# Optimization experiments

Hardware: AMD Instinct MI355X
Metric: run time of the kernel (lower is better)

## Reference

```python
import jax, jax.numpy as jnp
import numpy as np

VOCAB_SIZE = 8192
EMBED_DIM = 256


def setup_inputs() -> dict:
    key = jax.random.key(0)
    k1, k2 = jax.random.split(key)
    N = 16384  # batch(512) * num_slots(8) * tokens_per_slot(4)
    z = jax.random.normal(k1, (N, EMBED_DIM), dtype=jnp.float32)
    codebook = jax.random.normal(k2, (VOCAB_SIZE, EMBED_DIM), dtype=jnp.float32)
    return {"z": z, "codebook": codebook}


def reference(z, codebook):
    # Squared-distance cdist via the expansion ||z||^2 + ||e||^2 - 2 z.e^T
    z_sq = jnp.sum(z * z, axis=1, keepdims=True)            # [N, 1]
    e_sq = jnp.sum(codebook * codebook, axis=1)              # [V]
    dist = z_sq + e_sq - 2.0 * jnp.matmul(z, codebook.T)     # [N, V]
    tokens = jnp.argmin(dist, axis=-1)                       # [N] int
    z_q = codebook[tokens]                                   # [N, E] gather
    # one-hot reference count (side statistic in the original forward)
    ref_count = jnp.zeros((VOCAB_SIZE,), dtype=jnp.float32).at[tokens].add(1.0)
    return tokens, z_q, ref_count
```

## Files before the change

### kernel.cpp

```cpp
#include <hip/hip_runtime.h>
#include <math.h>

#define N_ROWS 16384
#define VOCAB  8192
#define EMB    256

#define BM 128
#define BV 128
#define BK 64
#define VSPLIT 8
#define VRANGE (VOCAB / VSPLIT)
#define NVT    (VRANGE / BV)
#define TAU 0.15f

typedef _Float16 half8 __attribute__((ext_vector_type(8)));
typedef _Float16 half4 __attribute__((ext_vector_type(4)));
typedef float floatx4 __attribute__((ext_vector_type(4)));

__device__ __forceinline__ void load_lds16(const _Float16* g, _Float16* l) {
    __builtin_amdgcn_global_load_lds(
        (const __attribute__((address_space(1))) void*)g,
        (__attribute__((address_space(3))) void*)l, 16, 0, 0);
}

__global__ void prep_kernel(const float* __restrict__ z, const float* __restrict__ cb,
                            _Float16* __restrict__ zh, _Float16* __restrict__ ch,
                            float* __restrict__ esq, float* __restrict__ cnt,
                            unsigned long long* __restrict__ rkey,
                            int* __restrict__ flagcnt) {
    const int b = blockIdx.x, t = threadIdx.x;
    if (b < VOCAB / 4) {
        const int row  = b * 4 + (t >> 6);
        const int lane = t & 63;
        const float4 f = *(const float4*)(cb + (size_t)row * EMB + lane * 4);
        half4 h;
        h.x = (_Float16)f.x; h.y = (_Float16)f.y; h.z = (_Float16)f.z; h.w = (_Float16)f.w;
        *(half4*)(ch + (size_t)row * EMB + lane * 4) = h;
        float s = f.x * f.x + f.y * f.y + f.z * f.z + f.w * f.w;
        #pragma unroll
        for (int off = 32; off > 0; off >>= 1) s += __shfl_down(s, off, 64);
        if (lane == 0) esq[row] = s;
        if (t < 4) cnt[b * 4 + t] = 0.0f;
        if (t >= 8 && t < 16) rkey[b * 8 + (t - 8)] = ~0ull;
        if (b == 0 && t == 4) flagcnt[0] = 0;
        if (b == 0 && t == 5) flagcnt[1] = 0;
    } else {
        const size_t idx4 = (size_t)(b - VOCAB / 4) * 256 + t;
        const float4 f = *(const float4*)(z + idx4 * 4);
        half4 h;
        h.x = (_Float16)f.x; h.y = (_Float16)f.y; h.z = (_Float16)f.z; h.w = (_Float16)f.w;
        *(half4*)(zh + idx4 * 4) = h;
    }
}

#define KSTEP(KT, RD, WR, LASTSTEP)                                            \
    {                                                                          \
        if (!(LASTSTEP)) {                                                     \
            const _Float16* csn_ = ((KT) < 3) ? csrc : (csrc + (size_t)BV * EMB); \
            const int kon_ = (((KT) + 1) & 3) * BK;                            \
            _Pragma("unroll")                                                  \
            for (int q = 0; q < 4; ++q) {                                      \
                load_lds16(zsrc + (size_t)q * 8 * EMB + kon_,                  \
                           &zs[WR][w * 2048 + q * 512]);                       \
                load_lds16(csn_ + (size_t)q * 8 * EMB + kon_,                  \
                           &cs[WR][w * 2048 + q * 512]);                       \
            }                                                                  \
            asm volatile("s_waitcnt vmcnt(8)" ::: "memory");                   \
        } else {                                                               \
            asm volatile("s_waitcnt vmcnt(0)" ::: "memory");                   \
        }                                                                      \
        __builtin_amdgcn_s_barrier();                                          \
        _Pragma("unroll")                                                      \
        for (int s_ = 0; s_ < 2; ++s_) {                                       \
            const int off_ = s_ ? offA1 : offA0;                               \
            half8 a_[4];                                                       \
            _Pragma("unroll")                                                  \
            for (int i_ = 0; i_ < 4; ++i_)                                     \
                a_[i_] = *(const half8*)&zs[RD][rA[i_] + off_];                \
            _Pragma("unroll")                                                  \
            for (int j_ = 0; j_ < 4; ++j_) {                                   \
                const half8 b_ = *(const half8*)&cs[RD][rB[j_] + off_];        \
                _Pragma("unroll")                                              \
                for (int i_ = 0; i_ < 4; ++i_)                                 \
                    acc[i_][j_] = __builtin_amdgcn_mfma_f32_16x16x32_f16(      \
                        a_[i_], b_, acc[i_][j_], 0, 0, 0);                     \
            }                                                                  \
        }                                                                      \
        __builtin_amdgcn_s_barrier();                                          \
    }

__global__ __launch_bounds__(256, 2)
void mfma_dist_kernel(const _Float16* __restrict__ zh, const _Float16* __restrict__ ch,
                      const float* __restrict__ esq,
                      float* __restrict__ pd1, float* __restrict__ pd2,
                      float* __restrict__ pd3,
                      int* __restrict__ pi1, int* __restrict__ pi2) {
    __shared__ _Float16 zs[2][BM * BK];
    __shared__ _Float16 cs[2][BV * BK];
    float* sc_d1 = (float*)zs;
    float* sc_d2 = sc_d1 + BM * 2;
    float* sc_d3 = sc_d2 + BM * 2;
    int*   sc_i1 = (int*)(sc_d3 + BM * 2);
    int*   sc_i2 = sc_i1 + BM * 2;

    const int row0  = blockIdx.x * BM;
    const int vbase = blockIdx.y * VRANGE;

    const int tid  = threadIdx.x;
    const int w    = tid >> 6;
    const int lane = tid & 63;
    const int lr   = lane & 15;
    const int quad = lane >> 4;
    const int mh   = (w >> 1) * 64;
    const int vh   = (w & 1) * 64;

    const int q7   = quad ^ (lr & 7);
    const int offA0 = q7 * 8;
    const int offA1 = (4 ^ q7) * 8;
    int rA[4], rB[4];
    #pragma unroll
    for (int i = 0; i < 4; ++i) { rA[i] = (mh + i * 16 + lr) * BK; rB[i] = (vh + i * 16 + lr) * BK; }

    const int schunk = (lane & 7) ^ (lane >> 3);
    const _Float16* zsrc = zh + (size_t)(row0 + w * 32 + (lane >> 3)) * EMB + schunk * 8;

    float m1[16], m2[16], m3[16]; int i1[16], i2[16];
    #pragma unroll
    for (int t = 0; t < 16; ++t) {
        m1[t] = -INFINITY; m2[t] = -INFINITY; m3[t] = -INFINITY; i1[t] = 0; i2[t] = 0;
    }

    float ev[4];
    #pragma unroll
    for (int j = 0; j < 4; ++j) ev[j] = esq[vbase + vh + j * 16 + lr];

    {
        const _Float16* csrc0 = ch + (size_t)(vbase + w * 32 + (lane >> 3)) * EMB + schunk * 8;
        #pragma unroll
        for (int q = 0; q < 4; ++q) {
            load_lds16(zsrc  + (size_t)q * 8 * EMB, &zs[0][w * 2048 + q * 512]);
            load_lds16(csrc0 + (size_t)q * 8 * EMB, &cs[0][w * 2048 + q * 512]);
        }
    }

    for (int vt = 0; vt < NVT; ++vt) {
        const int v0 = vbase + vt * BV;
        const _Float16* csrc = ch + (size_t)(v0 + w * 32 + (lane >> 3)) * EMB + schunk * 8;

        floatx4 acc[4][4];
        #pragma unroll
        for (int j = 0; j < 4; ++j) {
            const float e2 = -0.5f * ev[j];
            #pragma unroll
            for (int i = 0; i < 4; ++i) acc[i][j] = (floatx4)e2;
        }
        float evn[4];
        {
            const int vtn = (vt + 1 < NVT) ? vt + 1 : vt;
            #pragma unroll
            for (int j = 0; j < 4; ++j) evn[j] = esq[vbase + vtn * BV + vh + j * 16 + lr];
        }

        KSTEP(0, 0, 1, false)
        KSTEP(1, 1, 0, false)
        KSTEP(2, 0, 1, false)
        KSTEP(3, 1, 0, (vt == NVT - 1))

        int vj[4];
        #pragma unroll
        for (int j = 0; j < 4; ++j) vj[j] = v0 + vh + j * 16 + lr;
        #pragma unroll
        for (int i = 0; i < 4; ++i) {
            #pragma unroll
            for (int reg = 0; reg < 4; ++reg) {
                const int t = i * 4 + reg;
                #pragma unroll
                for (int j = 0; j < 4; ++j) {
                    const float a = acc[i][j][reg];
                    const bool gt1 = a > m1[t];
                    const bool gt2 = a > m2[t];
                    const bool gt3 = a > m3[t];
                    m3[t] = gt2 ? m2[t] : (gt3 ? a : m3[t]);
                    m2[t] = gt1 ? m1[t] : (gt2 ? a : m2[t]);
                    i2[t] = gt1 ? i1[t] : (gt2 ? vj[j] : i2[t]);
                    m1[t] = gt1 ? a : m1[t];
                    i1[t] = gt1 ? vj[j] : i1[t];
                }
            }
        }
        #pragma unroll
        for (int j = 0; j < 4; ++j) ev[j] = evn[j];
    }

    #pragma unroll
    for (int t = 0; t < 16; ++t) {
        float a1 = m1[t], a2 = m2[t], a3 = m3[t]; int ii1 = i1[t], ii2 = i2[t];
        #pragma unroll
        for (int off = 1; off < 16; off <<= 1) {
            const float o1 = __shfl_xor(a1, off, 64);
            const float o2 = __shfl_xor(a2, off, 64);
            const float o3 = __shfl_xor(a3, off, 64);
            const int  oi1 = __shfl_xor(ii1, off, 64);
            const int  oi2 = __shfl_xor(ii2, off, 64);
            const bool g1 = o1 > a1, g2 = o1 > a2, g3 = o1 > a3;
            a3  = g2 ? a2  : (g3 ? o1  : a3);
            a2  = g1 ? a1  : (g2 ? o1  : a2);
            ii2 = g1 ? ii1 : (g2 ? oi1 : ii2);
            a1  = g1 ? o1  : a1;
            ii1 = g1 ? oi1 : ii1;
            const bool h2 = o2 > a2, h3 = o2 > a3;
            a3  = h2 ? a2  : (h3 ? o2 : a3);
            a2  = h2 ? o2  : a2;
            ii2 = h2 ? oi2 : ii2;
            a3 = fmaxf(a3, o3);
        }
        m1[t] = a1; m2[t] = a2; m3[t] = a3; i1[t] = ii1; i2[t] = ii2;
    }
    if (lr == 0) {
        #pragma unroll
        for (int t = 0; t < 16; ++t) {
            const int r = mh + (t >> 2) * 16 + quad * 4 + (t & 3);
            sc_d1[r * 2 + (w & 1)] = m1[t];
            sc_d2[r * 2 + (w & 1)] = m2[t];
            sc_d3[r * 2 + (w & 1)] = m3[t];
            sc_i1[r * 2 + (w & 1)] = i1[t];
            sc_i2[r * 2 + (w & 1)] = i2[t];
        }
    }
    __syncthreads();
    if (tid < BM) {
        float a1 = sc_d1[tid * 2], a2 = sc_d2[tid * 2], a3 = sc_d3[tid * 2];
        int  ii1 = sc_i1[tid * 2], ii2 = sc_i2[tid * 2];
        const float o1 = sc_d1[tid * 2 + 1], o2 = sc_d2[tid * 2 + 1], o3 = sc_d3[tid * 2 + 1];
        const int  oi1 = sc_i1[tid * 2 + 1], oi2 = sc_i2[tid * 2 + 1];
        {
            const bool g1 = o1 > a1, g2 = o1 > a2, g3 = o1 > a3;
            a3  = g2 ? a2  : (g3 ? o1  : a3);
            a2  = g1 ? a1  : (g2 ? o1  : a2);
            ii2 = g1 ? ii1 : (g2 ? oi1 : ii2);
            a1  = g1 ? o1  : a1;
            ii1 = g1 ? oi1 : ii1;
            const bool h2 = o2 > a2, h3 = o2 > a3;
            a3  = h2 ? a2  : (h3 ? o2 : a3);
            a2  = h2 ? o2  : a2;
            ii2 = h2 ? oi2 : ii2;
            a3 = fmaxf(a3, o3);
        }
        const size_t o = (size_t)blockIdx.y * N_ROWS + row0 + tid;
        pd1[o] = -2.0f * a1; pd2[o] = -2.0f * a2; pd3[o] = -2.0f * a3;
        pi1[o] = ii1; pi2[o] = ii2;
    }
}
#undef KSTEP

__global__ void combine_kernel(const float* __restrict__ pd1, const float* __restrict__ pd2,
                               const float* __restrict__ pd3, const int* __restrict__ pi1,
                               const float* __restrict__ cb,
                               float* __restrict__ tokens, float* __restrict__ zq,
                               float* __restrict__ cnt,
                               int* __restrict__ flagcnt,
                               int* __restrict__ clist, int* __restrict__ flist) {
    const int wave = threadIdx.x >> 6;
    const int lane = threadIdx.x & 63;
    const int row  = blockIdx.x * 4 + wave;

    float g1 = INFINITY, g2 = INFINITY, mind3 = INFINITY; int gi = 0;
    #pragma unroll
    for (int s = 0; s < VSPLIT; ++s) {
        const size_t o = (size_t)s * N_ROWS + row;
        const float od1 = pd1[o], od2 = pd2[o], od3 = pd3[o]; const int oi1 = pi1[o];
        if (od1 < g1) { g2 = fminf(g1, od2); g1 = od1; gi = oi1; }
        else          { g2 = fminf(g2, od1); }
        mind3 = fminf(mind3, od3);
    }
    if ((g2 - g1) < TAU) {
        if (lane == 0) {
            if (mind3 >= g1 + TAU) {
                const int pos = atomicAdd(&flagcnt[0], 1);
                clist[pos] = row;
            } else {
                const int pos = atomicAdd(&flagcnt[1], 1);
                flist[pos] = row;
            }
        }
        return;
    }
    if (lane == 0) {
        tokens[row] = (float)gi;
        atomicAdd(&cnt[gi], 1.0f);
    }
    const float4 v = *(const float4*)(cb + (size_t)gi * EMB + lane * 4);
    *(float4*)(zq + (size_t)row * EMB + lane * 4) = v;
}

__global__ void rescue_cand_kernel(const int* __restrict__ flagcnt,
                                   const int* __restrict__ clist,
                                   const float* __restrict__ z, const float* __restrict__ cb,
                                   const float* __restrict__ esq,
                                   const int* __restrict__ pi1, const int* __restrict__ pi2,
                                   float* __restrict__ tokens, float* __restrict__ zq,
                                   float* __restrict__ cnt) {
    const int n    = flagcnt[0];
    const int w    = threadIdx.x >> 6;
    const int lane = threadIdx.x & 63;
    const int c    = lane >> 2;
    const int s    = lane & 3;

    for (int f = blockIdx.x * 4 + w; f < n; f += gridDim.x * 4) {
        const int row = clist[f];
        const size_t po = (size_t)(c & 7) * N_ROWS + row;
        const int cidx = (c < 8) ? pi1[po] : pi2[po];

        const float* zr = z  + (size_t)row  * EMB + s * 64;
        const float* cr = cb + (size_t)cidx * EMB + s * 64;
        float p0 = 0.0f, p1 = 0.0f, p2 = 0.0f, p3 = 0.0f;
        #pragma unroll
        for (int k = 0; k < 4; ++k) {
            const float4 z0 = *(const float4*)(zr + k * 16 + 0);
            const float4 c0 = *(const float4*)(cr + k * 16 + 0);
            const float4 z1 = *(const float4*)(zr + k * 16 + 4);
            const float4 c1 = *(const float4*)(cr + k * 16 + 4);
            const float4 z2 = *(const float4*)(zr + k * 16 + 8);
            const float4 c2 = *(const float4*)(cr + k * 16 + 8);
            const float4 z3 = *(const float4*)(zr + k * 16 + 12);
            const float4 c3 = *(const float4*)(cr + k * 16 + 12);
            p0 += z0.x * c0.x + z0.y * c0.y + z0.z * c0.z + z0.w * c0.w;
            p1 += z1.x * c1.x + z1.y * c1.y + z1.z * c1.z + z1.w * c1.w;
            p2 += z2.x * c2.x + z2.y * c2.y + z2.z * c2.z + z2.w * c2.w;
            p3 += z3.x * c3.x + z3.y * c3.y + z3.z * c3.z + z3.w * c3.w;
        }
        float p = (p0 + p1) + (p2 + p3);
        p += __shfl_xor(p, 1, 64);
        p += __shfl_xor(p, 2, 64);

        float bd = esq[cidx] - 2.0f * p;
        int   bv = cidx;
        #pragma unroll
        for (int off = 4; off < 64; off <<= 1) {
            const float od = __shfl_xor(bd, off, 64);
            const int   ov = __shfl_xor(bv, off, 64);
            if (od < bd || (od == bd && ov < bv)) { bd = od; bv = ov; }
        }
        if (lane == 0) {
            tokens[row] = (float)bv;
            atomicAdd(&cnt[bv], 1.0f);
        }
        const float4 c4 = *(const float4*)(cb + (size_t)bv * EMB + lane * 4);
        *(float4*)(zq + (size_t)row * EMB + lane * 4) = c4;
    }
}

#define RBV 64
#define RSPLIT 4
#define NTILE (VOCAB / RBV)
__global__ __launch_bounds__(256, 2)
void rescue_full_kernel(const int* __restrict__ flagcnt, const int* __restrict__ flist,
                        const float* __restrict__ z, const float* __restrict__ cb,
                        const float* __restrict__ esq,
                        unsigned long long* __restrict__ rkey) {
    const int n = __builtin_amdgcn_readfirstlane(flagcnt[1]);
    if (n == 0) return;

    __shared__ float cs[RBV][EMB];

    const int tile = blockIdx.x >> 2;
    const int rs   = blockIdx.x & 3;
    const int c0   = tile * RBV;
    const int tid  = threadIdx.x;
    const int w    = tid >> 6;
    const int lane = tid & 63;
    const int g    = lane >> 2;
    const int s    = lane & 3;

    #pragma unroll
    for (int i = 0; i < 16; ++i) {
        const int code = i * 4 + w;
        const float4 v = *(const float4*)(cb + (size_t)(c0 + code) * EMB + lane * 4);
        *(float4*)&cs[code][(lane ^ (code & 7)) * 4] = v;
    }
    __syncthreads();

    const int nq = (n + 3) >> 2;
    const int q0 = (rs << 2) | w;
    if (q0 >= nq) return;

    float ev[4];
    #pragma unroll
    for (int gs = 0; gs < 4; ++gs) ev[gs] = esq[c0 + gs * 16 + g];

    for (int q = q0; q < nq; q += 16) {
        int rows[4];
        #pragma unroll
        for (int r = 0; r < 4; ++r) {
            const int fi = q * 4 + r;
            rows[r] = __builtin_amdgcn_readfirstlane(flist[fi < n ? fi : 0]);
        }

        float p[4][4];
        #pragma unroll
        for (int gs = 0; gs < 4; ++gs)
            #pragma unroll
            for (int r = 0; r < 4; ++r) p[gs][r] = 0.0f;

        #pragma unroll
        for (int kb = 0; kb < 4; ++kb) {
            #pragma unroll
            for (int kk = 0; kk < 4; ++kk) {
                const int dbase = (kb * 4 + kk) * 16 + s * 4;
                float4 zv[4];
                #pragma unroll
                for (int r = 0; r < 4; ++r)
                    zv[r] = *(const float4*)(z + (size_t)rows[r] * EMB + dbase);
                const int dq = (kb * 4 + kk) * 4 + s;
                #pragma unroll
                for (int gs = 0; gs < 4; ++gs) {
                    const int code = gs * 16 + g;
                    const float4 c4 = *(const float4*)&cs[code][(dq ^ (code & 7)) * 4];
                    #pragma unroll
                    for (int r = 0; r < 4; ++r)
                        p[gs][r] += zv[r].x * c4.x + zv[r].y * c4.y
                                  + zv[r].z * c4.z + zv[r].w * c4.w;
                }
            }
        }

        #pragma unroll
        for (int gs = 0; gs < 4; ++gs)
            #pragma unroll
            for (int r = 0; r < 4; ++r) {
                float t = p[gs][r];
                t += __shfl_xor(t, 1, 64);
                t += __shfl_xor(t, 2, 64);
                p[gs][r] = t;
            }

        #pragma unroll
        for (int r = 0; r < 4; ++r) {
            float bd = INFINITY; int bv = 0;
            #pragma unroll
            for (int gs = 0; gs < 4; ++gs) {
                const float d = ev[gs] - 2.0f * p[gs][r];
                const int v = c0 + gs * 16 + g;
                if (d < bd) { bd = d; bv = v; }
            }
            #pragma unroll
            for (int off = 4; off < 64; off <<= 1) {
                const float od = __shfl_xor(bd, off, 64);
                const int   ov = __shfl_xor(bv, off, 64);
                if (od < bd || (od == bd && ov < bv)) { bd = od; bv = ov; }
            }
            if (lane == 0 && q * 4 + r < n) {
                unsigned int u = __float_as_uint(bd);
                u = (u & 0x80000000u) ? ~u : (u | 0x80000000u);
                atomicMin(rkey + rows[r], ((unsigned long long)u << 32) | (unsigned int)bv);
            }
        }
    }
}

__global__ void rescue_write_kernel(const int* __restrict__ flagcnt,
                                    const int* __restrict__ flist,
                                    const unsigned long long* __restrict__ rkey,
                                    const float* __restrict__ cb,
                                    float* __restrict__ tokens, float* __restrict__ zq,
                                    float* __restrict__ cnt) {
    const int w    = threadIdx.x >> 6;
    const int lane = threadIdx.x & 63;
    const int n = flagcnt[1];
    for (int f = blockIdx.x * 4 + w; f < n; f += gridDim.x * 4) {
        const int row = flist[f];
        const int v = (int)(unsigned int)(rkey[row] & 0xFFFFFFFFull);
        if (lane == 0) {
            tokens[row] = (float)v;
            atomicAdd(&cnt[v], 1.0f);
        }
        const float4 c4 = *(const float4*)(cb + (size_t)v * EMB + lane * 4);
        *(float4*)(zq + (size_t)row * EMB + lane * 4) = c4;
    }
}

__global__ void esq_kernel(const float* __restrict__ cb, float* __restrict__ esq) {
    const int wave = threadIdx.x >> 6;
    const int lane = threadIdx.x & 63;
    const int row  = blockIdx.x * 4 + wave;
    const float4 v = *(const float4*)(cb + (size_t)row * EMB + lane * 4);
    float s = v.x * v.x + v.y * v.y + v.z * v.z + v.w * v.w;
    #pragma unroll
    for (int off = 32; off > 0; off >>= 1) s += __shfl_down(s, off, 64);
    if (lane == 0) esq[row] = s;
}

#define FLSTR 36
__global__ __launch_bounds__(256, 2)
void fb_dist_kernel(const float* __restrict__ z, const float* __restrict__ cb,
                    const float* __restrict__ esq,
                    float* __restrict__ pdist, int* __restrict__ pidx) {
    __shared__ float zs[BM][FLSTR];
    __shared__ float es[BV][FLSTR];
    __shared__ float rdist[16][16];
    __shared__ int   ridx [16][16];
    const int row0 = blockIdx.x * BM, vbase = blockIdx.y * VRANGE;
    const int tid = threadIdx.x, wave = tid >> 6, lane = tid & 63;
    const int wly = (lane >> 3) & 7, wlx = lane & 7;
    const int wbase = (wave >> 1) * 64, cbase = (wave & 1) * 64;
    const int arow = wbase + wly, bcol = cbase + wlx;
    const int rowSlot = (wave >> 1) * 8 + wly, colSlot = (wave & 1) * 8 + wlx;
    const int sc4 = tid & 7, sr0 = tid >> 3;
    float best[8]; int bidx[8];
    #pragma unroll
    for (int i = 0; i < 8; ++i) { best[i] = INFINITY; bidx[i] = 0; }
    for (int vt = 0; vt < NVT; ++vt) {
        const int v0 = vbase + vt * BV;
        float acc[8][8];
        #pragma unroll
        for (int i = 0; i < 8; ++i)
            #pragma unroll
            for (int j = 0; j < 8; ++j) acc[i][j] = 0.0f;
        #pragma unroll 1
        for (int kt = 0; kt < EMB / 32; ++kt) {
            #pragma unroll
            for (int t = 0; t < 4; ++t) {
                const int r = sr0 + 32 * t;
                *(float4*)&zs[r][sc4 * 4] = *(const float4*)(z  + (size_t)(row0 + r) * EMB + kt * 32 + sc4 * 4);
                *(float4*)&es[r][sc4 * 4] = *(const float4*)(cb + (size_t)(v0 + r) * EMB + kt * 32 + sc4 * 4);
            }
            __syncthreads();
            #pragma unroll 1
            for (int k0 = 0; k0 < 8; ++k0) {
                const int kk = k0 * 4;
                float a[8][4];
                #pragma unroll
                for (int i = 0; i < 8; ++i) {
                    const float4 a4 = *(const float4*)&zs[arow + 8 * i][kk];
                    a[i][0] = a4.x; a[i][1] = a4.y; a[i][2] = a4.z; a[i][3] = a4.w;
                }
                #pragma unroll
                for (int j = 0; j < 8; ++j) {
                    const float4 b4 = *(const float4*)&es[bcol + 8 * j][kk];
                    #pragma unroll
                    for (int i = 0; i < 8; ++i) {
                        acc[i][j] += a[i][0] * b4.x; acc[i][j] += a[i][1] * b4.y;
                        acc[i][j] += a[i][2] * b4.z; acc[i][j] += a[i][3] * b4.w;
                    }
                }
            }
            __syncthreads();
        }
        #pragma unroll
        for (int j = 0; j < 8; ++j) {
            const int v = v0 + bcol + 8 * j;
            const float evv = esq[v];
            #pragma unroll
            for (int i = 0; i < 8; ++i) {
                const float d = evv - 2.0f * acc[i][j];
                if (d < best[i]) { best[i] = d; bidx[i] = v; }
            }
        }
    }
    for (int i = 0; i < 8; ++i) {
        rdist[rowSlot][colSlot] = best[i];
        ridx [rowSlot][colSlot] = bidx[i];
        __syncthreads();
        if (colSlot == 0) {
            float bd = rdist[rowSlot][0]; int bi = ridx[rowSlot][0];
            #pragma unroll
            for (int t = 1; t < 16; ++t) {
                const float d = rdist[rowSlot][t]; const int ii = ridx[rowSlot][t];
                if (d < bd || (d == bd && ii < bi)) { bd = d; bi = ii; }
            }
            const int row = row0 + wbase + 8 * i + wly;
            pdist[(size_t)blockIdx.y * N_ROWS + row] = bd;
            pidx [(size_t)blockIdx.y * N_ROWS + row] = bi;
        }
        __syncthreads();
    }
}

__global__ void fb_combine_kernel(const float* __restrict__ pdist, const int* __restrict__ pidx,
                                  const float* __restrict__ cb,
                                  float* __restrict__ tokens, float* __restrict__ zq,
                                  float* __restrict__ cnt) {
    const int wave = threadIdx.x >> 6, lane = threadIdx.x & 63;
    const int row = blockIdx.x * 4 + wave;
    float bd = INFINITY; int bi = 0;
    #pragma unroll
    for (int s = 0; s < VSPLIT; ++s) {
        const float d = pdist[(size_t)s * N_ROWS + row];
        const int ii  = pidx [(size_t)s * N_ROWS + row];
        if (d < bd || (d == bd && ii < bi)) { bd = d; bi = ii; }
    }
    if (lane == 0) { tokens[row] = (float)bi; atomicAdd(&cnt[bi], 1.0f); }
    const float4 v = *(const float4*)(cb + (size_t)bi * EMB + lane * 4);
    *(float4*)(zq + (size_t)row * EMB + lane * 4) = v;
}

extern "C" void kernel_launch(void* const* d_in, const int* in_sizes, int n_in,
                              void* d_out, int out_size, void* d_ws, size_t ws_size,
                              hipStream_t stream) {
    const float* z  = (const float*)d_in[0];
    const float* cb = (const float*)d_in[1];

    float* out    = (float*)d_out;
    float* tokens = out;
    float* zq     = out + N_ROWS;
    float* cnt    = out + N_ROWS + (size_t)N_ROWS * EMB;

    const size_t ZE = (size_t)N_ROWS * EMB, CE = (size_t)VOCAB * EMB, P = (size_t)VSPLIT * N_ROWS;
    const size_t NEED = (ZE + CE) * sizeof(_Float16) + VOCAB * 4
                      + 5 * P * 4 + (size_t)N_ROWS * 8 + 256 + 2 * (size_t)N_ROWS * 4;

    if (ws_size >= NEED) {
        char* p = (char*)d_ws;
        _Float16* zh = (_Float16*)p;            p += ZE * 2;
        _Float16* ch = (_Float16*)p;            p += CE * 2;
        float* esq   = (float*)p;               p += VOCAB * 4;
        float* pd1   = (float*)p;               p += P * 4;
        float* pd2   = (float*)p;               p += P * 4;
        float* pd3   = (float*)p;               p += P * 4;
        int*   pi1   = (int*)p;                 p += P * 4;
        int*   pi2   = (int*)p;                 p += P * 4;
        unsigned long long* rkey = (unsigned long long*)p;  p += (size_t)N_ROWS * 8;
        int*   flagcnt = (int*)p;               p += 256;
        int*   clist = (int*)p;                 p += (size_t)N_ROWS * 4;
        int*   flist = (int*)p;

        prep_kernel<<<VOCAB / 4 + (int)(ZE / 4 / 256), 256, 0, stream>>>(
            z, cb, zh, ch, esq, cnt, rkey, flagcnt);
        mfma_dist_kernel<<<dim3(N_ROWS / BM, VSPLIT), 256, 0, stream>>>(
            zh, ch, esq, pd1, pd2, pd3, pi1, pi2);
        combine_kernel<<<N_ROWS / 4, 256, 0, stream>>>(
            pd1, pd2, pd3, pi1, cb, tokens, zq, cnt, flagcnt, clist, flist);
        rescue_cand_kernel<<<512, 256, 0, stream>>>(
            flagcnt, clist, z, cb, esq, pi1, pi2, tokens, zq, cnt);
        rescue_full_kernel<<<NTILE * RSPLIT, 256, 0, stream>>>(
            flagcnt, flist, z, cb, esq, rkey);
        rescue_write_kernel<<<32, 256, 0, stream>>>(
            flagcnt, flist, rkey, cb, tokens, zq, cnt);
    } else {
        float* esq   = (float*)d_ws;
        float* pdist = esq + VOCAB;
        int*   pidx  = (int*)(pdist + P);
        hipMemsetAsync(cnt, 0, VOCAB * sizeof(float), stream);
        esq_kernel<<<VOCAB / 4, 256, 0, stream>>>(cb, esq);
        fb_dist_kernel<<<dim3(N_ROWS / BM, VSPLIT), 256, 0, stream>>>(z, cb, esq, pdist, pidx);
        fb_combine_kernel<<<N_ROWS / 4, 256, 0, stream>>>(pdist, pidx, cb, tokens, zq, cnt);
    }
}
```

Before: 210.5 us.

## Pack code index into distance bits, simplify pipeline barriers, merge rescue kernels

The top-3 tracking in the distance kernel now embeds the tile and column index in the low 5 mantissa bits of each score. That lets a branchless fmin/fmax network replace the compare-and-select logic, and indices are recovered from the bits after the loop. The k-step pipeline swaps explicit waitcnt plus two raw barriers for a single __syncthreads before issuing the next stage loads. The candidate and full rescue kernels are fused into one launch with a block-range split. Together these cut VALU work and launch overhead, at the cost of slightly perturbed scores and a possibly weaker load/compute overlap.

```diff
diff --git a/kernel.cpp b/kernel.cpp
--- a/kernel.cpp
+++ b/kernel.cpp
@@ -53,23 +53,19 @@
     }
 }
 
-#define KSTEP(KT, RD, WR, LASTSTEP)                                            \
+#define KSTEP(RD, WR, NKO, NCS, DOSTAGE)                                       \
     {                                                                          \
-        if (!(LASTSTEP)) {                                                     \
-            const _Float16* csn_ = ((KT) < 3) ? csrc : (csrc + (size_t)BV * EMB); \
-            const int kon_ = (((KT) + 1) & 3) * BK;                            \
+        __syncthreads();                                                       \
+        if (DOSTAGE) {                                                         \
+            const _Float16* ncs_ = (NCS);                                      \
             _Pragma("unroll")                                                  \
             for (int q = 0; q < 4; ++q) {                                      \
-                load_lds16(zsrc + (size_t)q * 8 * EMB + kon_,                  \
+                load_lds16(zsrc + (size_t)q * 8 * EMB + (NKO),                 \
                            &zs[WR][w * 2048 + q * 512]);                       \
-                load_lds16(csn_ + (size_t)q * 8 * EMB + kon_,                  \
+                load_lds16(ncs_ + (size_t)q * 8 * EMB + (NKO),                 \
                            &cs[WR][w * 2048 + q * 512]);                       \
             }                                                                  \
-            asm volatile("s_waitcnt vmcnt(8)" ::: "memory");                   \
-        } else {                                                               \
-            asm volatile("s_waitcnt vmcnt(0)" ::: "memory");                   \
         }                                                                      \
-        __builtin_amdgcn_s_barrier();                                          \
         _Pragma("unroll")                                                      \
         for (int s_ = 0; s_ < 2; ++s_) {                                       \
             const int off_ = s_ ? offA1 : offA0;                               \
@@ -86,7 +82,6 @@
                         a_[i_], b_, acc[i_][j_], 0, 0, 0);                     \
             }                                                                  \
         }                                                                      \
-        __builtin_amdgcn_s_barrier();                                          \
     }
 
 __global__ __launch_bounds__(256, 2)
@@ -124,11 +119,9 @@
     const int schunk = (lane & 7) ^ (lane >> 3);
     const _Float16* zsrc = zh + (size_t)(row0 + w * 32 + (lane >> 3)) * EMB + schunk * 8;
 
-    float m1[16], m2[16], m3[16]; int i1[16], i2[16];
-    #pragma unroll
-    for (int t = 0; t < 16; ++t) {
-        m1[t] = -INFINITY; m2[t] = -INFINITY; m3[t] = -INFINITY; i1[t] = 0; i2[t] = 0;
-    }
+    float m1[16], m2[16], m3[16];
+    #pragma unroll
+    for (int t = 0; t < 16; ++t) { m1[t] = -INFINITY; m2[t] = -INFINITY; m3[t] = -INFINITY; }
 
     float ev[4];
     #pragma unroll
@@ -161,14 +154,11 @@
             for (int j = 0; j < 4; ++j) evn[j] = esq[vbase + vtn * BV + vh + j * 16 + lr];
         }
 
-        KSTEP(0, 0, 1, false)
-        KSTEP(1, 1, 0, false)
-        KSTEP(2, 0, 1, false)
-        KSTEP(3, 1, 0, (vt == NVT - 1))
-
-        int vj[4];
-        #pragma unroll
-        for (int j = 0; j < 4; ++j) vj[j] = v0 + vh + j * 16 + lr;
+        KSTEP(0, 1, BK,     csrc, true)
+        KSTEP(1, 0, 2 * BK, csrc, true)
+        KSTEP(0, 1, 3 * BK, csrc, true)
+        KSTEP(1, 0, 0,      csrc + (size_t)BV * EMB, (vt < NVT - 1))
+
         #pragma unroll
         for (int i = 0; i < 4; ++i) {
             #pragma unroll
@@ -176,20 +166,28 @@
                 const int t = i * 4 + reg;
                 #pragma unroll
                 for (int j = 0; j < 4; ++j) {
-                    const float a = acc[i][j][reg];
-                    const bool gt1 = a > m1[t];
-                    const bool gt2 = a > m2[t];
-                    const bool gt3 = a > m3[t];
-                    m3[t] = gt2 ? m2[t] : (gt3 ? a : m3[t]);
-                    m2[t] = gt1 ? m1[t] : (gt2 ? a : m2[t]);
-                    i2[t] = gt1 ? i1[t] : (gt2 ? vj[j] : i2[t]);
-                    m1[t] = gt1 ? a : m1[t];
-                    i1[t] = gt1 ? vj[j] : i1[t];
+                    const unsigned code = ((unsigned)vt << 2) | (unsigned)j;
+                    const float a = __uint_as_float(
+                        (__float_as_uint(acc[i][j][reg]) & ~31u) | code);
+                    const float mid = fminf(m1[t], a);
+                    m1[t] = fmaxf(m1[t], a);
+                    const float lo  = fminf(m2[t], mid);
+                    m2[t] = fmaxf(m2[t], mid);
+                    m3[t] = fmaxf(m3[t], lo);
                 }
             }
         }
         #pragma unroll
         for (int j = 0; j < 4; ++j) ev[j] = evn[j];
+    }
+
+    int i1[16], i2[16];
+    #pragma unroll
+    for (int t = 0; t < 16; ++t) {
+        const unsigned c1 = __float_as_uint(m1[t]) & 31u;
+        const unsigned c2 = __float_as_uint(m2[t]) & 31u;
+        i1[t] = vbase + (int)(c1 >> 2) * BV + vh + (int)(c1 & 3u) * 16 + lr;
+        i2[t] = vbase + (int)(c2 >> 2) * BV + vh + (int)(c2 & 3u) * 16 + lr;
     }
 
     #pragma unroll
@@ -293,82 +291,82 @@
     *(float4*)(zq + (size_t)row * EMB + lane * 4) = v;
 }
 
-__global__ void rescue_cand_kernel(const int* __restrict__ flagcnt,
-                                   const int* __restrict__ clist,
-                                   const float* __restrict__ z, const float* __restrict__ cb,
-                                   const float* __restrict__ esq,
-                                   const int* __restrict__ pi1, const int* __restrict__ pi2,
-                                   float* __restrict__ tokens, float* __restrict__ zq,
-                                   float* __restrict__ cnt) {
-    const int n    = flagcnt[0];
-    const int w    = threadIdx.x >> 6;
-    const int lane = threadIdx.x & 63;
-    const int c    = lane >> 2;
-    const int s    = lane & 3;
-
-    for (int f = blockIdx.x * 4 + w; f < n; f += gridDim.x * 4) {
-        const int row = clist[f];
-        const size_t po = (size_t)(c & 7) * N_ROWS + row;
-        const int cidx = (c < 8) ? pi1[po] : pi2[po];
-
-        const float* zr = z  + (size_t)row  * EMB + s * 64;
-        const float* cr = cb + (size_t)cidx * EMB + s * 64;
-        float p0 = 0.0f, p1 = 0.0f, p2 = 0.0f, p3 = 0.0f;
-        #pragma unroll
-        for (int k = 0; k < 4; ++k) {
-            const float4 z0 = *(const float4*)(zr + k * 16 + 0);
-            const float4 c0 = *(const float4*)(cr + k * 16 + 0);
-            const float4 z1 = *(const float4*)(zr + k * 16 + 4);
-            const float4 c1 = *(const float4*)(cr + k * 16 + 4);
-            const float4 z2 = *(const float4*)(zr + k * 16 + 8);
-            const float4 c2 = *(const float4*)(cr + k * 16 + 8);
-            const float4 z3 = *(const float4*)(zr + k * 16 + 12);
-            const float4 c3 = *(const float4*)(cr + k * 16 + 12);
-            p0 += z0.x * c0.x + z0.y * c0.y + z0.z * c0.z + z0.w * c0.w;
-            p1 += z1.x * c1.x + z1.y * c1.y + z1.z * c1.z + z1.w * c1.w;
-            p2 += z2.x * c2.x + z2.y * c2.y + z2.z * c2.z + z2.w * c2.w;
-            p3 += z3.x * c3.x + z3.y * c3.y + z3.z * c3.z + z3.w * c3.w;
-        }
-        float p = (p0 + p1) + (p2 + p3);
-        p += __shfl_xor(p, 1, 64);
-        p += __shfl_xor(p, 2, 64);
-
-        float bd = esq[cidx] - 2.0f * p;
-        int   bv = cidx;
-        #pragma unroll
-        for (int off = 4; off < 64; off <<= 1) {
-            const float od = __shfl_xor(bd, off, 64);
-            const int   ov = __shfl_xor(bv, off, 64);
-            if (od < bd || (od == bd && ov < bv)) { bd = od; bv = ov; }
-        }
-        if (lane == 0) {
-            tokens[row] = (float)bv;
-            atomicAdd(&cnt[bv], 1.0f);
-        }
-        const float4 c4 = *(const float4*)(cb + (size_t)bv * EMB + lane * 4);
-        *(float4*)(zq + (size_t)row * EMB + lane * 4) = c4;
-    }
-}
-
 #define RBV 64
 #define RSPLIT 4
 #define NTILE (VOCAB / RBV)
+#define CAND_BLOCKS 128
 __global__ __launch_bounds__(256, 2)
-void rescue_full_kernel(const int* __restrict__ flagcnt, const int* __restrict__ flist,
-                        const float* __restrict__ z, const float* __restrict__ cb,
-                        const float* __restrict__ esq,
-                        unsigned long long* __restrict__ rkey) {
-    const int n = __builtin_amdgcn_readfirstlane(flagcnt[1]);
-    if (n == 0) return;
-
-    __shared__ float cs[RBV][EMB];
-
-    const int tile = blockIdx.x >> 2;
-    const int rs   = blockIdx.x & 3;
-    const int c0   = tile * RBV;
+void rescue_kernel(const int* __restrict__ flagcnt,
+                   const int* __restrict__ clist, const int* __restrict__ flist,
+                   const float* __restrict__ z, const float* __restrict__ cb,
+                   const float* __restrict__ esq,
+                   const int* __restrict__ pi1, const int* __restrict__ pi2,
+                   float* __restrict__ tokens, float* __restrict__ zq,
+                   float* __restrict__ cnt,
+                   unsigned long long* __restrict__ rkey) {
+    __shared__ float csf[RBV][EMB];
+
     const int tid  = threadIdx.x;
     const int w    = tid >> 6;
     const int lane = tid & 63;
+
+    if (blockIdx.x < CAND_BLOCKS) {
+        const int n = flagcnt[0];
+        const int c = lane >> 2;
+        const int s = lane & 3;
+
+        for (int f = blockIdx.x * 4 + w; f < n; f += CAND_BLOCKS * 4) {
+            const int row = clist[f];
+            const size_t po = (size_t)(c & 7) * N_ROWS + row;
+            const int cidx = (c < 8) ? pi1[po] : pi2[po];
+
+            const float* zr = z  + (size_t)row  * EMB + s * 64;
+            const float* cr = cb + (size_t)cidx * EMB + s * 64;
+            float p0 = 0.0f, p1 = 0.0f, p2 = 0.0f, p3 = 0.0f;
+            #pragma unroll
+            for (int k = 0; k < 4; ++k) {
+                const float4 z0 = *(const float4*)(zr + k * 16 + 0);
+                const float4 c0 = *(const float4*)(cr + k * 16 + 0);
+                const float4 z1 = *(const float4*)(zr + k * 16 + 4);
+                const float4 c1 = *(const float4*)(cr + k * 16 + 4);
+                const float4 z2 = *(const float4*)(zr + k * 16 + 8);
+                const float4 c2 = *(const float4*)(cr + k * 16 + 8);
+                const float4 z3 = *(const float4*)(zr + k * 16 + 12);
+                const float4 c3 = *(const float4*)(cr + k * 16 + 12);
+                p0 += z0.x * c0.x + z0.y * c0.y + z0.z * c0.z + z0.w * c0.w;
+                p1 += z1.x * c1.x + z1.y * c1.y + z1.z * c1.z + z1.w * c1.w;
+                p2 += z2.x * c2.x + z2.y * c2.y + z2.z * c2.z + z2.w * c2.w;
+                p3 += z3.x * c3.x + z3.y * c3.y + z3.z * c3.z + z3.w * c3.w;
+            }
+            float p = (p0 + p1) + (p2 + p3);
+            p += __shfl_xor(p, 1, 64);
+            p += __shfl_xor(p, 2, 64);
+
+            float bd = esq[cidx] - 2.0f * p;
+            int   bv = cidx;
+            #pragma unroll
+            for (int off = 4; off < 64; off <<= 1) {
+                const float od = __shfl_xor(bd, off, 64);
+                const int   ov = __shfl_xor(bv, off, 64);
+                if (od < bd || (od == bd && ov < bv)) { bd = od; bv = ov; }
+            }
+            if (lane == 0) {
+                tokens[row] = (float)bv;
+                atomicAdd(&cnt[bv], 1.0f);
+            }
+            const float4 c4 = *(const float4*)(cb + (size_t)bv * EMB + lane * 4);
+            *(float4*)(zq + (size_t)row * EMB + lane * 4) = c4;
+        }
+        return;
+    }
+
+    const int n = __builtin_amdgcn_readfirstlane(flagcnt[1]);
+    if (n == 0) return;
+
+    const int bid  = blockIdx.x - CAND_BLOCKS;
+    const int tile = bid >> 2;
+    const int rs   = bid & 3;
+    const int c0   = tile * RBV;
     const int g    = lane >> 2;
     const int s    = lane & 3;
 
@@ -376,7 +374,7 @@
     for (int i = 0; i < 16; ++i) {
         const int code = i * 4 + w;
         const float4 v = *(const float4*)(cb + (size_t)(c0 + code) * EMB + lane * 4);
-        *(float4*)&cs[code][(lane ^ (code & 7)) * 4] = v;
+        *(float4*)&csf[code][(lane ^ (code & 7)) * 4] = v;
     }
     __syncthreads();
 
@@ -415,7 +413,7 @@
                 #pragma unroll
                 for (int gs = 0; gs < 4; ++gs) {
                     const int code = gs * 16 + g;
-                    const float4 c4 = *(const float4*)&cs[code][(dq ^ (code & 7)) * 4];
+                    const float4 c4 = *(const float4*)&csf[code][(dq ^ (code & 7)) * 4];
                     #pragma unroll
                     for (int r = 0; r < 4; ++r)
                         p[gs][r] += zv[r].x * c4.x + zv[r].y * c4.y
@@ -630,10 +628,8 @@
             zh, ch, esq, pd1, pd2, pd3, pi1, pi2);
         combine_kernel<<<N_ROWS / 4, 256, 0, stream>>>(
             pd1, pd2, pd3, pi1, cb, tokens, zq, cnt, flagcnt, clist, flist);
-        rescue_cand_kernel<<<512, 256, 0, stream>>>(
-            flagcnt, clist, z, cb, esq, pi1, pi2, tokens, zq, cnt);
-        rescue_full_kernel<<<NTILE * RSPLIT, 256, 0, stream>>>(
-            flagcnt, flist, z, cb, esq, rkey);
+        rescue_kernel<<<CAND_BLOCKS + NTILE * RSPLIT, 256, 0, stream>>>(
+            flagcnt, clist, flist, z, cb, esq, pi1, pi2, tokens, zq, cnt, rkey);
         rescue_write_kernel<<<32, 256, 0, stream>>>(
             flagcnt, flist, rkey, cb, tokens, zq, cnt);
     } else {
```

Measured after the change: 201.4 us. -4.3%, faster.
